# Performance work log

Hardware: AMD Instinct MI355X
Metric: run time of the kernel (lower is better)

## Reference

```python
import jax, jax.numpy as jnp
import numpy as np

N = 50000      # nodes
E = 800000     # edges (before self-loops)
H = 4          # heads
C = 32         # hidden per head (hidden*heads = 128); out_channels = 32
IN = 128
NEG_SLOPE = 0.2


def setup_inputs() -> dict:
    key = jax.random.key(0)
    ks = jax.random.split(key, 16)
    s = 0.1
    d = {
        "x": jax.random.normal(ks[0], (N, IN), jnp.float32),
        "edge_index": jax.random.randint(ks[1], (2, E), 0, N),
        "edge_type": jax.random.randint(ks[2], (E,), 0, 38),
        "node_type": jax.random.randint(ks[3], (N,), 0, 4),
        # layer 1: in=128 -> H*C, concat
        "W1": jax.random.normal(ks[4], (IN, H * C), jnp.float32) * s,
        "a1s": jax.random.normal(ks[5], (H, C), jnp.float32) * s,
        "a1d": jax.random.normal(ks[6], (H, C), jnp.float32) * s,
        "b1": jnp.zeros((H * C,), jnp.float32),
        # layer 2: H*C -> H*C, concat
        "W2": jax.random.normal(ks[7], (H * C, H * C), jnp.float32) * s,
        "a2s": jax.random.normal(ks[8], (H, C), jnp.float32) * s,
        "a2d": jax.random.normal(ks[9], (H, C), jnp.float32) * s,
        "b2": jnp.zeros((H * C,), jnp.float32),
        # layer 3: H*C -> C, heads=1, mean (concat=False)
        "W3": jax.random.normal(ks[10], (H * C, C), jnp.float32) * s,
        "a3s": jax.random.normal(ks[11], (1, C), jnp.float32) * s,
        "a3d": jax.random.normal(ks[12], (1, C), jnp.float32) * s,
        "b3": jnp.zeros((C,), jnp.float32),
    }
    return d


def gat_layer(x, src, dst, W, a_s, a_d, b, heads, concat):
    # PyG GATConv (eval mode): linear, per-edge attention logits, segment
    # softmax over incoming edges at dst, weighted scatter-sum, bias.
    h = (x @ W).reshape(N, heads, -1)            # [N, H, C]
    al_s = jnp.einsum('nhc,hc->nh', h, a_s)       # [N, H]
    al_d = jnp.einsum('nhc,hc->nh', h, a_d)
    e = jax.nn.leaky_relu(al_s[src] + al_d[dst], NEG_SLOPE)   # [E', H]
    m = jax.ops.segment_max(e, dst, num_segments=N)            # [N, H]
    p = jnp.exp(e - m[dst])
    z = jax.ops.segment_sum(p, dst, num_segments=N)            # [N, H]
    alpha = p / (z[dst] + 1e-16)                               # [E', H]
    out = jax.ops.segment_sum(h[src] * alpha[..., None], dst, num_segments=N)  # [N, H, C]
    out = out.reshape(N, -1) if concat else out.mean(axis=1)
    return out + b


def reference(x, edge_index, edge_type, node_type,
              W1, a1s, a1d, b1, W2, a2s, a2d, b2, W3, a3s, a3d, b3):
    # add self-loops (PyG GATConv default add_self_loops=True)
    loop = jnp.arange(N, dtype=edge_index.dtype)
    src = jnp.concatenate([edge_index[0], loop])
    dst = jnp.concatenate([edge_index[1], loop])
    h = gat_layer(x, src, dst, W1, a1s, a1d, b1, H, True)
    h = jax.nn.elu(h)
    h = gat_layer(h, src, dst, W2, a2s, a2d, b2, H, True)
    h = jax.nn.elu(h)
    out = gat_layer(h, src, dst, W3, a3s, a3d, b3, 1, False)
    return out
```

## Files before the change

### kernel.cpp

```cpp
#include <hip/hip_runtime.h>
#include <hip/hip_fp16.h>

#define LRELU_SLOPE 0.2f
#define BSH 8
#define EPB 3584
#define BCAP 5120
#define NSH 6

typedef _Float16 f16x8 __attribute__((ext_vector_type(8)));
typedef float f32x4 __attribute__((ext_vector_type(4)));

__device__ __forceinline__ float lrelu(float x) { return x >= 0.0f ? x : LRELU_SLOPE * x; }

__device__ __forceinline__ float sel4(float a, float b, float c, float d, int h) {
  float r = a;
  r = (h == 1) ? b : r;
  r = (h == 2) ? c : r;
  r = (h == 3) ? d : r;
  return r;
}


__device__ __forceinline__ void prep_one(const float* __restrict__ W, __half* __restrict__ out,
                                         int NT, int t) {
  int l = t & 63, f = t >> 6;
  int kt = f / NT, nt = f % NT;
  int k0 = kt * 32 + (l >> 4) * 8;
  int col = nt * 16 + (l & 15);
  union { __half h[8]; float4 v; } u;
#pragma unroll
  for (int j = 0; j < 8; ++j) u.h[j] = (__half)W[(size_t)(k0 + j) * (NT * 16) + col];
  *(float4*)(out + (size_t)t * 8) = u.v;
}

__global__ __launch_bounds__(256) void k_init(
    int* __restrict__ gcur,
    const float* __restrict__ W1, __half* __restrict__ wf1,
    const float* __restrict__ W2, __half* __restrict__ wf2,
    const float* __restrict__ W3, __half* __restrict__ wf3) {
  if (blockIdx.x == 0) {
    gcur[threadIdx.x] = threadIdx.x * BCAP;
    return;
  }
  int t = (blockIdx.x - 1) * 256 + threadIdx.x;
  if (t < 2048) prep_one(W1, wf1, 8, t);
  else if (t < 4096) prep_one(W2, wf2, 8, t - 2048);
  else if (t < 4608) prep_one(W3, wf3, 2, t - 4096);
}


__device__ __forceinline__ f16x8 load_a(const float* xp) {
  float4 lo = *(const float4*)xp;
  float4 hi = *(const float4*)(xp + 4);
  f16x8 a;
  a[0] = (_Float16)lo.x; a[1] = (_Float16)lo.y; a[2] = (_Float16)lo.z; a[3] = (_Float16)lo.w;
  a[4] = (_Float16)hi.x; a[5] = (_Float16)hi.y; a[6] = (_Float16)hi.z; a[7] = (_Float16)hi.w;
  return a;
}

__device__ __forceinline__ f16x8 load_a(const __half* xp) {
  return *(const f16x8*)xp;
}

template <int NT, int NH, typename IN, typename OUT>
__device__ __forceinline__ void gemm_body(
    const IN* __restrict__ x, const __half* __restrict__ wfrag,
    const float* __restrict__ a_s, const float* __restrict__ a_d,
    OUT* __restrict__ h, float* __restrict__ als, float* __restrict__ ald,
    int n, int ntiles, int tile, int lane) {
  const f16x8* wf = (const f16x8*)wfrag;
  f16x8 B[4][NT];
#pragma unroll
  for (int kt = 0; kt < 4; ++kt)
#pragma unroll
    for (int nt = 0; nt < NT; ++nt) B[kt][nt] = wf[(kt * NT + nt) * 64 + lane];
  if (tile >= ntiles) return;
  int r0 = tile * 16;
  int arow = r0 + (lane & 15);
  const IN* xp = x + (size_t)arow * 128 + (lane >> 4) * 8;
  bool full = (r0 + 16 <= n);
  f16x8 A[4];
#pragma unroll
  for (int kt = 0; kt < 4; ++kt) {
    if (full || arow < n) A[kt] = load_a(xp + kt * 32);
    else A[kt] = (f16x8){};
  }
  f32x4 acc[NT];
#pragma unroll
  for (int nt = 0; nt < NT; ++nt) acc[nt] = (f32x4){0.f, 0.f, 0.f, 0.f};
#pragma unroll
  for (int kt = 0; kt < 4; ++kt)
#pragma unroll
    for (int nt = 0; nt < NT; ++nt)
      acc[nt] = __builtin_amdgcn_mfma_f32_16x16x32_f16(A[kt], B[kt][nt], acc[nt], 0, 0, 0);
  int cb = lane & 15, rb = (lane >> 4) * 4;
  float asv[NT], adv[NT];
#pragma unroll
  for (int nt = 0; nt < NT; ++nt) {
    asv[nt] = a_s[nt * 16 + cb];
    adv[nt] = a_d[nt * 16 + cb];
  }
#pragma unroll
  for (int r = 0; r < 4; ++r) {
    int row = r0 + rb + r;
    if (!full && row >= n) break;
#pragma unroll
    for (int nt = 0; nt < NT; ++nt)
      h[(size_t)row * (NT * 16) + nt * 16 + cb] = (OUT)acc[nt][r];
    if (NH == 4) {
      float ps[4], pd[4];
#pragma unroll
      for (int hh = 0; hh < 4; ++hh) {
        ps[hh] = acc[2 * hh][r] * asv[2 * hh] + acc[2 * hh + 1][r] * asv[2 * hh + 1];
        pd[hh] = acc[2 * hh][r] * adv[2 * hh] + acc[2 * hh + 1][r] * adv[2 * hh + 1];
      }
#pragma unroll
      for (int off = 1; off < 16; off <<= 1) {
#pragma unroll
        for (int hh = 0; hh < 4; ++hh) {
          ps[hh] += __shfl_xor(ps[hh], off);
          pd[hh] += __shfl_xor(pd[hh], off);
        }
      }
      if (cb < 4) {
        als[row * 4 + cb] = sel4(ps[0], ps[1], ps[2], ps[3], cb);
        ald[row * 4 + cb] = sel4(pd[0], pd[1], pd[2], pd[3], cb);
      }
    } else {
      float ps = acc[0][r] * asv[0] + acc[1][r] * asv[1];
      float pd = acc[0][r] * adv[0] + acc[1][r] * adv[1];
#pragma unroll
      for (int off = 1; off < 16; off <<= 1) {
        ps += __shfl_xor(ps, off);
        pd += __shfl_xor(pd, off);
      }
      if (cb == 0) { als[row] = ps; ald[row] = pd; }
    }
  }
}

template <int NT, int NH, typename IN, typename OUT>
__global__ __launch_bounds__(256, 2) void gemm_mfma(
    const IN* __restrict__ x, const __half* __restrict__ wfrag,
    const float* __restrict__ a_s, const float* __restrict__ a_d,
    OUT* __restrict__ h, float* __restrict__ als, float* __restrict__ ald,
    int n, int ntiles) {
  int lane = threadIdx.x & 63, w = threadIdx.x >> 6;
  gemm_body<NT, NH, IN, OUT>(x, wfrag, a_s, a_d, h, als, ald, n, ntiles,
                             blockIdx.x * 4 + w, lane);
}


__global__ __launch_bounds__(256) void k_bucket_gemm(
    const int* __restrict__ ei, int E, int* __restrict__ gcur, int* __restrict__ ebuck,
    int bblocks,
    const float* __restrict__ x, const __half* __restrict__ wf1,
    const float* __restrict__ a1s, const float* __restrict__ a1d,
    __half* __restrict__ hA, float* __restrict__ als, float* __restrict__ ald,
    int n, int ntiles) {
  __shared__ int stage[EPB];
  __shared__ unsigned char bucket8[EPB];
  __shared__ int cnt[256], offs[256], gbase[256], curl[256], sm[256];
  if (blockIdx.x >= bblocks) {
    int lane = threadIdx.x & 63, w = threadIdx.x >> 6;
    gemm_body<8, 4, float, __half>(x, wf1, a1s, a1d, hA, als, ald, n, ntiles,
                                   (blockIdx.x - bblocks) * 4 + w, lane);
    return;
  }
  int t = threadIdx.x;
  int base = blockIdx.x * EPB;
  int count = E - base;
  if (count > EPB) count = EPB;
  if (count < 0) count = 0;
  cnt[t] = 0;
  __syncthreads();
  for (int i = t; i < count; i += 256) {
    int d = ei[E + base + i];
    atomicAdd(&cnt[d >> BSH], 1);
  }
  __syncthreads();
  sm[t] = cnt[t];
  __syncthreads();
#pragma unroll
  for (int off = 1; off < 256; off <<= 1) {
    int u = (t >= off) ? sm[t - off] : 0;
    __syncthreads();
    sm[t] += u;
    __syncthreads();
  }
  offs[t] = sm[t] - cnt[t];
  curl[t] = sm[t] - cnt[t];
  if (cnt[t] > 0) gbase[t] = atomicAdd(&gcur[t], cnt[t]);
  __syncthreads();
  for (int i = t; i < count; i += 256) {
    int s = ei[base + i];
    int d = ei[E + base + i];
    int b = d >> BSH;
    int r = atomicAdd(&curl[b], 1);
    stage[r] = (s << 8) | (d & 255);
    bucket8[r] = (unsigned char)b;
  }
  __syncthreads();
  for (int i = t; i < count; i += 256) {
    int b = bucket8[i];
    ebuck[gbase[b] + (i - offs[b])] = stage[i];
  }
}


__global__ __launch_bounds__(256) void k_fine_gemm(
    const int* __restrict__ ebuck, const int* __restrict__ gcur,
    int* __restrict__ rowend, int* __restrict__ colx, int n, int fineBlocks,
    const float* __restrict__ x, const __half* __restrict__ wf1,
    const float* __restrict__ a1s, const float* __restrict__ a1d,
    __half* __restrict__ hA, float* __restrict__ als, float* __restrict__ ald,
    int ntiles, int tile0) {
  if (blockIdx.x >= fineBlocks) {
    int lane = threadIdx.x & 63, w = threadIdx.x >> 6;
    gemm_body<8, 4, float, __half>(x, wf1, a1s, a1d, hA, als, ald, n, ntiles,
                                   tile0 + (blockIdx.x - fineBlocks) * 4 + w, lane);
    return;
  }
  __shared__ int cur[256];
  int b = blockIdx.x, t = threadIdx.x;
  int lo = b << BSH;
  int hi = lo + 256;
  if (hi > n) hi = n;
  int nn = hi - lo;
  cur[t] = (lo + t) << NSH;
  __syncthreads();
  int ebeg = b * BCAP, eend = gcur[b];
  for (int i = ebeg + t; i < eend; i += 256) {
    int p = ebuck[i];
    int pos = atomicAdd(&cur[p & 255], 1);
    colx[pos] = p >> 8;
  }
  __syncthreads();
  if (t < nn) rowend[lo + t] = cur[t];
}


__global__ __launch_bounds__(256) void k_agg128(
    const __half* __restrict__ h, const float* __restrict__ als,
    const float* __restrict__ ald, const int* __restrict__ rowend,
    const int* __restrict__ colx, const float* __restrict__ bias,
    __half* __restrict__ out, int n) {
  int w = threadIdx.x >> 6, lane = threadIdx.x & 63;
  int node = blockIdx.x * 4 + w;
  if (node >= n) return;
  int g = lane >> 3, q = lane & 7, head = q >> 1;
  int beg = node << NSH, end = rowend[node];
  float adh = ald[node * 4 + head];
  float acc[16] = {};
  float z = 0.f;
  int c0 = q * 16;
  if (g == 0) {
    float ws = __expf(lrelu(als[node * 4 + head] + adh));
    z = ws;
    float4 ra = *(const float4*)(h + (size_t)node * 128 + c0);
    float4 rb = *(const float4*)(h + (size_t)node * 128 + c0 + 8);
    const __half2* ha = (const __half2*)&ra;
    const __half2* hb = (const __half2*)&rb;
#pragma unroll
    for (int j = 0; j < 4; ++j) {
      float2 fa = __half22float2(ha[j]);
      float2 fb = __half22float2(hb[j]);
      acc[2 * j] = ws * fa.x;
      acc[2 * j + 1] = ws * fa.y;
      acc[8 + 2 * j] = ws * fb.x;
      acc[8 + 2 * j + 1] = ws * fb.y;
    }
  }
  for (int e = beg + g; e < end; e += 8) {
    int s = colx[e];
    float wv = __expf(lrelu(als[s * 4 + head] + adh));
    float4 ra = *(const float4*)(h + (size_t)s * 128 + c0);
    float4 rb = *(const float4*)(h + (size_t)s * 128 + c0 + 8);
    const __half2* ha = (const __half2*)&ra;
    const __half2* hb = (const __half2*)&rb;
    z += wv;
#pragma unroll
    for (int j = 0; j < 4; ++j) {
      float2 fa = __half22float2(ha[j]);
      float2 fb = __half22float2(hb[j]);
      acc[2 * j] = fmaf(wv, fa.x, acc[2 * j]);
      acc[2 * j + 1] = fmaf(wv, fa.y, acc[2 * j + 1]);
      acc[8 + 2 * j] = fmaf(wv, fb.x, acc[8 + 2 * j]);
      acc[8 + 2 * j + 1] = fmaf(wv, fb.y, acc[8 + 2 * j + 1]);
    }
  }
#pragma unroll
  for (int off = 8; off <= 32; off <<= 1) {
    z += __shfl_xor(z, off);
#pragma unroll
    for (int j = 0; j < 16; ++j) acc[j] += __shfl_xor(acc[j], off);
  }
  if (g == 0) {
    float inv = 1.f / z;
    union { __half h8[8]; float4 v; } ua, ub;
#pragma unroll
    for (int j = 0; j < 8; ++j) {
      float va = acc[j] * inv + bias[c0 + j];
      va = (va > 0.f) ? va : (__expf(va) - 1.f);
      ua.h8[j] = (__half)va;
      float vb = acc[8 + j] * inv + bias[c0 + 8 + j];
      vb = (vb > 0.f) ? vb : (__expf(vb) - 1.f);
      ub.h8[j] = (__half)vb;
    }
    *(float4*)&out[(size_t)node * 128 + c0] = ua.v;
    *(float4*)&out[(size_t)node * 128 + c0 + 8] = ub.v;
  }
}


__global__ __launch_bounds__(256) void k_agg32(
    const __half* __restrict__ h, const float* __restrict__ als,
    const float* __restrict__ ald, const int* __restrict__ rowend,
    const int* __restrict__ colx, const float* __restrict__ bias,
    float* __restrict__ out, int n) {
  int w = threadIdx.x >> 6, lane = threadIdx.x & 63;
  int node = blockIdx.x * 4 + w;
  if (node >= n) return;
  int g = lane >> 3, q = lane & 7;
  int beg = node << NSH, end = rowend[node];
  float ad = ald[node];
  float acc[4] = {};
  float z = 0.f;
  int c0 = q * 4;
  if (g == 0) {
    float ws = __expf(lrelu(als[node] + ad));
    float2 raw = *(const float2*)(h + (size_t)node * 32 + c0);
    const __half2* hh = (const __half2*)&raw;
    z = ws;
#pragma unroll
    for (int j = 0; j < 2; ++j) {
      float2 f = __half22float2(hh[j]);
      acc[2 * j] = ws * f.x;
      acc[2 * j + 1] = ws * f.y;
    }
  }
  for (int e = beg + g; e < end; e += 8) {
    int s = colx[e];
    float wv = __expf(lrelu(als[s] + ad));
    float2 raw = *(const float2*)(h + (size_t)s * 32 + c0);
    const __half2* hh = (const __half2*)&raw;
    z += wv;
#pragma unroll
    for (int j = 0; j < 2; ++j) {
      float2 f = __half22float2(hh[j]);
      acc[2 * j] = fmaf(wv, f.x, acc[2 * j]);
      acc[2 * j + 1] = fmaf(wv, f.y, acc[2 * j + 1]);
    }
  }
#pragma unroll
  for (int off = 8; off <= 32; off <<= 1) {
    z += __shfl_xor(z, off);
#pragma unroll
    for (int j = 0; j < 4; ++j) acc[j] += __shfl_xor(acc[j], off);
  }
  if (g == 0) {
    float inv = 1.f / z;
    float4 o;
    o.x = acc[0] * inv + bias[c0];
    o.y = acc[1] * inv + bias[c0 + 1];
    o.z = acc[2] * inv + bias[c0 + 2];
    o.w = acc[3] * inv + bias[c0 + 3];
    *(float4*)&out[(size_t)node * 32 + c0] = o;
  }
}


extern "C" void kernel_launch(void* const* d_in, const int* in_sizes, int n_in,
                              void* d_out, int out_size, void* d_ws, size_t ws_size,
                              hipStream_t stream) {
  const float* x   = (const float*)d_in[0];
  const int*   ei  = (const int*)d_in[1];
  const float* W1  = (const float*)d_in[4];
  const float* a1s = (const float*)d_in[5];
  const float* a1d = (const float*)d_in[6];
  const float* b1  = (const float*)d_in[7];
  const float* W2  = (const float*)d_in[8];
  const float* a2s = (const float*)d_in[9];
  const float* a2d = (const float*)d_in[10];
  const float* b2  = (const float*)d_in[11];
  const float* W3  = (const float*)d_in[12];
  const float* a3s = (const float*)d_in[13];
  const float* a3d = (const float*)d_in[14];
  const float* b3  = (const float*)d_in[15];
  const int N = in_sizes[0] / 128;
  const int E = in_sizes[1] / 2;
  const int ntiles = (N + 15) / 16;
  const int nbuck = (N + 255) >> BSH;

  char* ws = (char*)d_ws;
  size_t off = 0;
  auto alloc = [&](size_t bytes) -> void* {
    void* p = ws + off;
    off += (bytes + 255) & ~(size_t)255;
    return p;
  };
  __half* hA    = (__half*)alloc((size_t)N * 128 * 2);
  __half* hB    = (__half*)alloc((size_t)N * 128 * 2);
  __half* h32   = (__half*)alloc((size_t)N * 32 * 2);
  float*  als_a = (float*)alloc((size_t)N * 4 * 4);
  float*  ald_a = (float*)alloc((size_t)N * 4 * 4);
  float*  als_b = (float*)alloc((size_t)N * 4 * 4);
  float*  ald_b = (float*)alloc((size_t)N * 4 * 4);
  float*  als1  = (float*)alloc((size_t)N * 4);
  float*  ald1  = (float*)alloc((size_t)N * 4);
  int* rowend   = (int*)alloc((size_t)N * 4);
  int* gcur     = (int*)alloc(256 * 4);
  int* ebuck    = (int*)alloc((size_t)nbuck * BCAP * 4);
  int* colx     = (int*)alloc(((size_t)N << NSH) * 4);
  __half* wf1   = (__half*)alloc(4 * 8 * 64 * 8 * 2);
  __half* wf2   = (__half*)alloc(4 * 8 * 64 * 8 * 2);
  __half* wf3   = (__half*)alloc(4 * 2 * 64 * 8 * 2);
  (void)ws_size; (void)n_in; (void)out_size;

  k_init<<<19, 256, 0, stream>>>(gcur, W1, wf1, W2, wf2, W3, wf3);

  int gblk = (ntiles + 3) / 4;
  int bblocks = (E + EPB - 1) / EPB;
  int g1a = (gblk * 3) / 5;
  int g1b = gblk - g1a;
  int tile0 = g1a * 4;

  k_bucket_gemm<<<bblocks + g1a, 256, 0, stream>>>(ei, E, gcur, ebuck, bblocks,
                                                   x, wf1, a1s, a1d, hA, als_a, ald_a,
                                                   N, ntiles);
  k_fine_gemm<<<nbuck + g1b, 256, 0, stream>>>(ebuck, gcur, rowend, colx, N, nbuck,
                                               x, wf1, a1s, a1d, hA, als_a, ald_a,
                                               ntiles, tile0);

  k_agg128<<<(N + 3) / 4, 256, 0, stream>>>(hA, als_a, ald_a, rowend, colx, b1, hB, N);
  gemm_mfma<8, 4, __half, __half><<<gblk, 256, 0, stream>>>(hB, wf2, a2s, a2d, hA,
                                                            als_b, ald_b, N, ntiles);
  k_agg128<<<(N + 3) / 4, 256, 0, stream>>>(hA, als_b, ald_b, rowend, colx, b2, hB, N);
  gemm_mfma<2, 1, __half, __half><<<gblk, 256, 0, stream>>>(hB, wf3, a3s, a3d, h32,
                                                            als1, ald1, N, ntiles);
  k_agg32<<<(N + 3) / 4, 256, 0, stream>>>(h32, als1, ald1, rowend, colx, b3,
                                           (float*)d_out, N);
}
```

Baseline: 156.2 us.

## Fuse attention aggregation with the following layer GEMM in one kernel

Replaces the separate aggregation and MFMA GEMM kernels for layers 2 and 3 with a fused kernel. Each 1024-thread block aggregates 16 nodes, one wave per node, into an LDS tile. It then runs the next layer's MFMA projection from LDS, splits K across two wave groups reduced through shared memory, and computes the attention logits for that layer. This removes the global write and re-read of the intermediate activations and two launches, at the cost of a large block size, extra syncthreads, and idle waves during the GEMM phase.

```diff
diff --git a/kernel.cpp b/kernel.cpp
--- a/kernel.cpp
+++ b/kernel.cpp
@@ -58,15 +58,11 @@
   return a;
 }
 
-__device__ __forceinline__ f16x8 load_a(const __half* xp) {
-  return *(const f16x8*)xp;
-}
-
-template <int NT, int NH, typename IN, typename OUT>
+template <int NT, int NH>
 __device__ __forceinline__ void gemm_body(
-    const IN* __restrict__ x, const __half* __restrict__ wfrag,
+    const float* __restrict__ x, const __half* __restrict__ wfrag,
     const float* __restrict__ a_s, const float* __restrict__ a_d,
-    OUT* __restrict__ h, float* __restrict__ als, float* __restrict__ ald,
+    __half* __restrict__ h, float* __restrict__ als, float* __restrict__ ald,
     int n, int ntiles, int tile, int lane) {
   const f16x8* wf = (const f16x8*)wfrag;
   f16x8 B[4][NT];
@@ -77,7 +73,7 @@
   if (tile >= ntiles) return;
   int r0 = tile * 16;
   int arow = r0 + (lane & 15);
-  const IN* xp = x + (size_t)arow * 128 + (lane >> 4) * 8;
+  const float* xp = x + (size_t)arow * 128 + (lane >> 4) * 8;
   bool full = (r0 + 16 <= n);
   f16x8 A[4];
 #pragma unroll
@@ -106,48 +102,26 @@
     if (!full && row >= n) break;
 #pragma unroll
     for (int nt = 0; nt < NT; ++nt)
-      h[(size_t)row * (NT * 16) + nt * 16 + cb] = (OUT)acc[nt][r];
-    if (NH == 4) {
-      float ps[4], pd[4];
+      h[(size_t)row * (NT * 16) + nt * 16 + cb] = (__half)acc[nt][r];
+    float ps[4], pd[4];
+#pragma unroll
+    for (int hh = 0; hh < 4; ++hh) {
+      ps[hh] = acc[2 * hh][r] * asv[2 * hh] + acc[2 * hh + 1][r] * asv[2 * hh + 1];
+      pd[hh] = acc[2 * hh][r] * adv[2 * hh] + acc[2 * hh + 1][r] * adv[2 * hh + 1];
+    }
+#pragma unroll
+    for (int off = 1; off < 16; off <<= 1) {
 #pragma unroll
       for (int hh = 0; hh < 4; ++hh) {
-        ps[hh] = acc[2 * hh][r] * asv[2 * hh] + acc[2 * hh + 1][r] * asv[2 * hh + 1];
-        pd[hh] = acc[2 * hh][r] * adv[2 * hh] + acc[2 * hh + 1][r] * adv[2 * hh + 1];
-      }
-#pragma unroll
-      for (int off = 1; off < 16; off <<= 1) {
-#pragma unroll
-        for (int hh = 0; hh < 4; ++hh) {
-          ps[hh] += __shfl_xor(ps[hh], off);
-          pd[hh] += __shfl_xor(pd[hh], off);
-        }
-      }
-      if (cb < 4) {
-        als[row * 4 + cb] = sel4(ps[0], ps[1], ps[2], ps[3], cb);
-        ald[row * 4 + cb] = sel4(pd[0], pd[1], pd[2], pd[3], cb);
-      }
-    } else {
-      float ps = acc[0][r] * asv[0] + acc[1][r] * asv[1];
-      float pd = acc[0][r] * adv[0] + acc[1][r] * adv[1];
-#pragma unroll
-      for (int off = 1; off < 16; off <<= 1) {
-        ps += __shfl_xor(ps, off);
-        pd += __shfl_xor(pd, off);
-      }
-      if (cb == 0) { als[row] = ps; ald[row] = pd; }
-    }
-  }
-}
-
-template <int NT, int NH, typename IN, typename OUT>
-__global__ __launch_bounds__(256, 2) void gemm_mfma(
-    const IN* __restrict__ x, const __half* __restrict__ wfrag,
-    const float* __restrict__ a_s, const float* __restrict__ a_d,
-    OUT* __restrict__ h, float* __restrict__ als, float* __restrict__ ald,
-    int n, int ntiles) {
-  int lane = threadIdx.x & 63, w = threadIdx.x >> 6;
-  gemm_body<NT, NH, IN, OUT>(x, wfrag, a_s, a_d, h, als, ald, n, ntiles,
-                             blockIdx.x * 4 + w, lane);
+        ps[hh] += __shfl_xor(ps[hh], off);
+        pd[hh] += __shfl_xor(pd[hh], off);
+      }
+    }
+    if (cb < 4) {
+      als[row * 4 + cb] = sel4(ps[0], ps[1], ps[2], ps[3], cb);
+      ald[row * 4 + cb] = sel4(pd[0], pd[1], pd[2], pd[3], cb);
+    }
+  }
 }
 
 
@@ -163,8 +137,8 @@
   __shared__ int cnt[256], offs[256], gbase[256], curl[256], sm[256];
   if (blockIdx.x >= bblocks) {
     int lane = threadIdx.x & 63, w = threadIdx.x >> 6;
-    gemm_body<8, 4, float, __half>(x, wf1, a1s, a1d, hA, als, ald, n, ntiles,
-                                   (blockIdx.x - bblocks) * 4 + w, lane);
+    gemm_body<8, 4>(x, wf1, a1s, a1d, hA, als, ald, n, ntiles,
+                    (blockIdx.x - bblocks) * 4 + w, lane);
     return;
   }
   int t = threadIdx.x;
@@ -217,8 +191,8 @@
     int ntiles, int tile0) {
   if (blockIdx.x >= fineBlocks) {
     int lane = threadIdx.x & 63, w = threadIdx.x >> 6;
-    gemm_body<8, 4, float, __half>(x, wf1, a1s, a1d, hA, als, ald, n, ntiles,
-                                   tile0 + (blockIdx.x - fineBlocks) * 4 + w, lane);
+    gemm_body<8, 4>(x, wf1, a1s, a1d, hA, als, ald, n, ntiles,
+                    tile0 + (blockIdx.x - fineBlocks) * 4 + w, lane);
     return;
   }
   __shared__ int cur[256];
@@ -240,75 +214,162 @@
 }
 
 
-__global__ __launch_bounds__(256) void k_agg128(
-    const __half* __restrict__ h, const float* __restrict__ als,
-    const float* __restrict__ ald, const int* __restrict__ rowend,
+template <int NT, int NHO>
+__global__ __launch_bounds__(1024, 8) void agg_gemm(
+    const __half* __restrict__ hin, const float* __restrict__ als_in,
+    const float* __restrict__ ald_in, const int* __restrict__ rowend,
     const int* __restrict__ colx, const float* __restrict__ bias,
-    __half* __restrict__ out, int n) {
-  int w = threadIdx.x >> 6, lane = threadIdx.x & 63;
-  int node = blockIdx.x * 4 + w;
-  if (node >= n) return;
+    const __half* __restrict__ wfrag, const float* __restrict__ a_s,
+    const float* __restrict__ a_d, __half* __restrict__ hout,
+    float* __restrict__ als_out, float* __restrict__ ald_out, int n) {
+  __shared__ _Float16 tile[16][136];
+  __shared__ float redbuf[NT][16][17];
+  __shared__ float lps[NT][16], lpd[NT][16];
+  int tid = threadIdx.x;
+  int wv = tid >> 6, lane = tid & 63;
+  int base = blockIdx.x * 16;
+  int node = base + wv;
   int g = lane >> 3, q = lane & 7, head = q >> 1;
-  int beg = node << NSH, end = rowend[node];
-  float adh = ald[node * 4 + head];
-  float acc[16] = {};
-  float z = 0.f;
   int c0 = q * 16;
-  if (g == 0) {
-    float ws = __expf(lrelu(als[node * 4 + head] + adh));
-    z = ws;
-    float4 ra = *(const float4*)(h + (size_t)node * 128 + c0);
-    float4 rb = *(const float4*)(h + (size_t)node * 128 + c0 + 8);
-    const __half2* ha = (const __half2*)&ra;
-    const __half2* hb = (const __half2*)&rb;
-#pragma unroll
-    for (int j = 0; j < 4; ++j) {
-      float2 fa = __half22float2(ha[j]);
-      float2 fb = __half22float2(hb[j]);
-      acc[2 * j] = ws * fa.x;
-      acc[2 * j + 1] = ws * fa.y;
-      acc[8 + 2 * j] = ws * fb.x;
-      acc[8 + 2 * j + 1] = ws * fb.y;
-    }
-  }
-  for (int e = beg + g; e < end; e += 8) {
-    int s = colx[e];
-    float wv = __expf(lrelu(als[s * 4 + head] + adh));
-    float4 ra = *(const float4*)(h + (size_t)s * 128 + c0);
-    float4 rb = *(const float4*)(h + (size_t)s * 128 + c0 + 8);
-    const __half2* ha = (const __half2*)&ra;
-    const __half2* hb = (const __half2*)&rb;
-    z += wv;
-#pragma unroll
-    for (int j = 0; j < 4; ++j) {
-      float2 fa = __half22float2(ha[j]);
-      float2 fb = __half22float2(hb[j]);
-      acc[2 * j] = fmaf(wv, fa.x, acc[2 * j]);
-      acc[2 * j + 1] = fmaf(wv, fa.y, acc[2 * j + 1]);
-      acc[8 + 2 * j] = fmaf(wv, fb.x, acc[8 + 2 * j]);
-      acc[8 + 2 * j + 1] = fmaf(wv, fb.y, acc[8 + 2 * j + 1]);
-    }
-  }
-#pragma unroll
-  for (int off = 8; off <= 32; off <<= 1) {
-    z += __shfl_xor(z, off);
-#pragma unroll
-    for (int j = 0; j < 16; ++j) acc[j] += __shfl_xor(acc[j], off);
-  }
-  if (g == 0) {
-    float inv = 1.f / z;
-    union { __half h8[8]; float4 v; } ua, ub;
-#pragma unroll
-    for (int j = 0; j < 8; ++j) {
-      float va = acc[j] * inv + bias[c0 + j];
-      va = (va > 0.f) ? va : (__expf(va) - 1.f);
-      ua.h8[j] = (__half)va;
-      float vb = acc[8 + j] * inv + bias[c0 + 8 + j];
-      vb = (vb > 0.f) ? vb : (__expf(vb) - 1.f);
-      ub.h8[j] = (__half)vb;
-    }
-    *(float4*)&out[(size_t)node * 128 + c0] = ua.v;
-    *(float4*)&out[(size_t)node * 128 + c0 + 8] = ub.v;
+
+  if (node < n) {
+    int beg = node << NSH, end = rowend[node];
+    float adh = ald_in[node * 4 + head];
+    float acc[16] = {};
+    float z = 0.f;
+    if (g == 0) {
+      float ws = __expf(lrelu(als_in[node * 4 + head] + adh));
+      z = ws;
+      float4 ra = *(const float4*)(hin + (size_t)node * 128 + c0);
+      float4 rb = *(const float4*)(hin + (size_t)node * 128 + c0 + 8);
+      const __half2* ha = (const __half2*)&ra;
+      const __half2* hb = (const __half2*)&rb;
+#pragma unroll
+      for (int j = 0; j < 4; ++j) {
+        float2 fa = __half22float2(ha[j]);
+        float2 fb = __half22float2(hb[j]);
+        acc[2 * j] = ws * fa.x;
+        acc[2 * j + 1] = ws * fa.y;
+        acc[8 + 2 * j] = ws * fb.x;
+        acc[8 + 2 * j + 1] = ws * fb.y;
+      }
+    }
+    for (int e = beg + g; e < end; e += 8) {
+      int s = colx[e];
+      float wv2 = __expf(lrelu(als_in[s * 4 + head] + adh));
+      float4 ra = *(const float4*)(hin + (size_t)s * 128 + c0);
+      float4 rb = *(const float4*)(hin + (size_t)s * 128 + c0 + 8);
+      const __half2* ha = (const __half2*)&ra;
+      const __half2* hb = (const __half2*)&rb;
+      z += wv2;
+#pragma unroll
+      for (int j = 0; j < 4; ++j) {
+        float2 fa = __half22float2(ha[j]);
+        float2 fb = __half22float2(hb[j]);
+        acc[2 * j] = fmaf(wv2, fa.x, acc[2 * j]);
+        acc[2 * j + 1] = fmaf(wv2, fa.y, acc[2 * j + 1]);
+        acc[8 + 2 * j] = fmaf(wv2, fb.x, acc[8 + 2 * j]);
+        acc[8 + 2 * j + 1] = fmaf(wv2, fb.y, acc[8 + 2 * j + 1]);
+      }
+    }
+#pragma unroll
+    for (int off = 8; off <= 32; off <<= 1) {
+      z += __shfl_xor(z, off);
+#pragma unroll
+      for (int j = 0; j < 16; ++j) acc[j] += __shfl_xor(acc[j], off);
+    }
+    if (g == 0) {
+      float inv = 1.f / z;
+      f16x8 oa, ob;
+#pragma unroll
+      for (int j = 0; j < 8; ++j) {
+        float va = acc[j] * inv + bias[c0 + j];
+        va = (va > 0.f) ? va : (__expf(va) - 1.f);
+        oa[j] = (_Float16)va;
+        float vb = acc[8 + j] * inv + bias[c0 + 8 + j];
+        vb = (vb > 0.f) ? vb : (__expf(vb) - 1.f);
+        ob[j] = (_Float16)vb;
+      }
+      *(f16x8*)&tile[wv][c0] = oa;
+      *(f16x8*)&tile[wv][c0 + 8] = ob;
+    }
+  } else if (g == 0) {
+    f16x8 zz = {};
+    *(f16x8*)&tile[wv][c0] = zz;
+    *(f16x8*)&tile[wv][c0 + 8] = zz;
+  }
+  __syncthreads();
+
+  constexpr int ACT = (NT == 8) ? 16 : 4;
+  bool active = wv < ACT;
+  int ct = (NT == 8) ? (wv & 7) : (wv & 1);
+  int kh = (NT == 8) ? (wv >> 3) : ((wv >> 1) & 1);
+  int cb = lane & 15, rb4 = (lane >> 4) * 4;
+  f32x4 acc2 = (f32x4){0.f, 0.f, 0.f, 0.f};
+  if (active) {
+    const f16x8* wf = (const f16x8*)wfrag;
+    int arow = lane & 15;
+    int koff = kh * 64 + (lane >> 4) * 8;
+#pragma unroll
+    for (int kt = 0; kt < 2; ++kt) {
+      f16x8 A = *(const f16x8*)&tile[arow][koff + kt * 32];
+      f16x8 B = wf[((kh * 2 + kt) * NT + ct) * 64 + lane];
+      acc2 = __builtin_amdgcn_mfma_f32_16x16x32_f16(A, B, acc2, 0, 0, 0);
+    }
+    if (kh == 1) {
+#pragma unroll
+      for (int r = 0; r < 4; ++r) redbuf[ct][rb4 + r][cb] = acc2[r];
+    }
+  }
+  __syncthreads();
+  if (active && kh == 0) {
+#pragma unroll
+    for (int r = 0; r < 4; ++r) acc2[r] += redbuf[ct][rb4 + r][cb];
+    float asv = a_s[ct * 16 + cb], adv = a_d[ct * 16 + cb];
+    bool full = (base + 16 <= n);
+    float ps[4], pd[4];
+#pragma unroll
+    for (int r = 0; r < 4; ++r) {
+      int row = base + rb4 + r;
+      if (full || row < n)
+        hout[(size_t)row * (NT * 16) + ct * 16 + cb] = (__half)acc2[r];
+      ps[r] = acc2[r] * asv;
+      pd[r] = acc2[r] * adv;
+    }
+#pragma unroll
+    for (int off = 1; off < 16; off <<= 1) {
+#pragma unroll
+      for (int r = 0; r < 4; ++r) {
+        ps[r] += __shfl_xor(ps[r], off);
+        pd[r] += __shfl_xor(pd[r], off);
+      }
+    }
+    if (cb == 0) {
+#pragma unroll
+      for (int r = 0; r < 4; ++r) {
+        lps[ct][rb4 + r] = ps[r];
+        lpd[ct][rb4 + r] = pd[r];
+      }
+    }
+  }
+  __syncthreads();
+  if (wv == 0) {
+    if (NHO == 4) {
+      int row = lane >> 2, h = lane & 3;
+      int nd = base + row;
+      if (nd < n) {
+        als_out[nd * 4 + h] = lps[2 * h][row] + lps[2 * h + 1][row];
+        ald_out[nd * 4 + h] = lpd[2 * h][row] + lpd[2 * h + 1][row];
+      }
+    } else {
+      if (lane < 16) {
+        int nd = base + lane;
+        if (nd < n) {
+          als_out[nd] = lps[0][lane] + lps[1][lane];
+          ald_out[nd] = lpd[0][lane] + lpd[1][lane];
+        }
+      }
+    }
   }
 }
 
@@ -400,7 +461,7 @@
     return p;
   };
   __half* hA    = (__half*)alloc((size_t)N * 128 * 2);
-  __half* hB    = (__half*)alloc((size_t)N * 128 * 2);
+  __half* hA2   = (__half*)alloc((size_t)N * 128 * 2);
   __half* h32   = (__half*)alloc((size_t)N * 32 * 2);
   float*  als_a = (float*)alloc((size_t)N * 4 * 4);
   float*  ald_a = (float*)alloc((size_t)N * 4 * 4);
@@ -432,12 +493,11 @@
                                                x, wf1, a1s, a1d, hA, als_a, ald_a,
                                                ntiles, tile0);
 
-  k_agg128<<<(N + 3) / 4, 256, 0, stream>>>(hA, als_a, ald_a, rowend, colx, b1, hB, N);
-  gemm_mfma<8, 4, __half, __half><<<gblk, 256, 0, stream>>>(hB, wf2, a2s, a2d, hA,
-                                                            als_b, ald_b, N, ntiles);
-  k_agg128<<<(N + 3) / 4, 256, 0, stream>>>(hA, als_b, ald_b, rowend, colx, b2, hB, N);
-  gemm_mfma<2, 1, __half, __half><<<gblk, 256, 0, stream>>>(hB, wf3, a3s, a3d, h32,
-                                                            als1, ald1, N, ntiles);
+  int fblk = (N + 15) / 16;
+  agg_gemm<8, 4><<<fblk, 1024, 0, stream>>>(hA, als_a, ald_a, rowend, colx, b1,
+                                            wf2, a2s, a2d, hA2, als_b, ald_b, N);
+  agg_gemm<2, 1><<<fblk, 1024, 0, stream>>>(hA2, als_b, ald_b, rowend, colx, b2,
+                                            wf3, a3s, a3d, h32, als1, ald1, N);
   k_agg32<<<(N + 3) / 4, 256, 0, stream>>>(h32, als1, ald1, rowend, colx, b3,
                                            (float*)d_out, N);
 }
```

New measurement: 170.8 us. +9.3%, slower.

## Store hidden features in 16-column slabs and split aggregation per slab

Applied to the files above, without the earlier changes.

Hidden features for layers 1 and 2 are now written as eight slabs, each holding a 16-column slice for all nodes. Attention logits move to a head-major layout. The 128-wide aggregation kernel is replaced by one that launches eight times as many blocks, each gathering one 32-byte slab row per edge, so the gathered working set per launch fits better in cache. In exchange, every block re-reads the edge list and logits and recomputes exp for its slab, which multiplies index and exp work by eight.

```diff
diff --git a/kernel.cpp b/kernel.cpp
--- a/kernel.cpp
+++ b/kernel.cpp
@@ -58,15 +58,11 @@
   return a;
 }
 
-__device__ __forceinline__ f16x8 load_a(const __half* xp) {
-  return *(const f16x8*)xp;
-}
-
-template <int NT, int NH, typename IN, typename OUT>
+template <int NT, int NH, bool SIN, bool SOUT, typename IN>
 __device__ __forceinline__ void gemm_body(
     const IN* __restrict__ x, const __half* __restrict__ wfrag,
     const float* __restrict__ a_s, const float* __restrict__ a_d,
-    OUT* __restrict__ h, float* __restrict__ als, float* __restrict__ ald,
+    __half* __restrict__ h, float* __restrict__ als, float* __restrict__ ald,
     int n, int ntiles, int tile, int lane) {
   const f16x8* wf = (const f16x8*)wfrag;
   f16x8 B[4][NT];
@@ -77,13 +73,22 @@
   if (tile >= ntiles) return;
   int r0 = tile * 16;
   int arow = r0 + (lane & 15);
-  const IN* xp = x + (size_t)arow * 128 + (lane >> 4) * 8;
   bool full = (r0 + 16 <= n);
+  bool rowok = full || arow < n;
+  int l4 = lane >> 4;
   f16x8 A[4];
 #pragma unroll
   for (int kt = 0; kt < 4; ++kt) {
-    if (full || arow < n) A[kt] = load_a(xp + kt * 32);
-    else A[kt] = (f16x8){};
+    if (rowok) {
+      if constexpr (SIN) {
+        const __half* hp = (const __half*)x;
+        A[kt] = *(const f16x8*)(hp + ((size_t)(kt * 2 + (l4 >> 1)) * n + arow) * 16 + (l4 & 1) * 8);
+      } else {
+        A[kt] = load_a(x + (size_t)arow * 128 + l4 * 8 + kt * 32);
+      }
+    } else {
+      A[kt] = (f16x8){};
+    }
   }
   f32x4 acc[NT];
 #pragma unroll
@@ -93,7 +98,7 @@
 #pragma unroll
     for (int nt = 0; nt < NT; ++nt)
       acc[nt] = __builtin_amdgcn_mfma_f32_16x16x32_f16(A[kt], B[kt][nt], acc[nt], 0, 0, 0);
-  int cb = lane & 15, rb = (lane >> 4) * 4;
+  int cb = lane & 15, rb = l4 * 4;
   float asv[NT], adv[NT];
 #pragma unroll
   for (int nt = 0; nt < NT; ++nt) {
@@ -105,8 +110,12 @@
     int row = r0 + rb + r;
     if (!full && row >= n) break;
 #pragma unroll
-    for (int nt = 0; nt < NT; ++nt)
-      h[(size_t)row * (NT * 16) + nt * 16 + cb] = (OUT)acc[nt][r];
+    for (int nt = 0; nt < NT; ++nt) {
+      if constexpr (SOUT)
+        h[((size_t)nt * n + row) * 16 + cb] = (__half)acc[nt][r];
+      else
+        h[(size_t)row * (NT * 16) + nt * 16 + cb] = (__half)acc[nt][r];
+    }
     if (NH == 4) {
       float ps[4], pd[4];
 #pragma unroll
@@ -123,8 +132,8 @@
         }
       }
       if (cb < 4) {
-        als[row * 4 + cb] = sel4(ps[0], ps[1], ps[2], ps[3], cb);
-        ald[row * 4 + cb] = sel4(pd[0], pd[1], pd[2], pd[3], cb);
+        als[(size_t)cb * n + row] = sel4(ps[0], ps[1], ps[2], ps[3], cb);
+        ald[(size_t)cb * n + row] = sel4(pd[0], pd[1], pd[2], pd[3], cb);
       }
     } else {
       float ps = acc[0][r] * asv[0] + acc[1][r] * asv[1];
@@ -139,15 +148,15 @@
   }
 }
 
-template <int NT, int NH, typename IN, typename OUT>
+template <int NT, int NH, bool SIN, bool SOUT, typename IN>
 __global__ __launch_bounds__(256, 2) void gemm_mfma(
     const IN* __restrict__ x, const __half* __restrict__ wfrag,
     const float* __restrict__ a_s, const float* __restrict__ a_d,
-    OUT* __restrict__ h, float* __restrict__ als, float* __restrict__ ald,
+    __half* __restrict__ h, float* __restrict__ als, float* __restrict__ ald,
     int n, int ntiles) {
   int lane = threadIdx.x & 63, w = threadIdx.x >> 6;
-  gemm_body<NT, NH, IN, OUT>(x, wfrag, a_s, a_d, h, als, ald, n, ntiles,
-                             blockIdx.x * 4 + w, lane);
+  gemm_body<NT, NH, SIN, SOUT, IN>(x, wfrag, a_s, a_d, h, als, ald, n, ntiles,
+                                   blockIdx.x * 4 + w, lane);
 }
 
 
@@ -163,8 +172,8 @@
   __shared__ int cnt[256], offs[256], gbase[256], curl[256], sm[256];
   if (blockIdx.x >= bblocks) {
     int lane = threadIdx.x & 63, w = threadIdx.x >> 6;
-    gemm_body<8, 4, float, __half>(x, wf1, a1s, a1d, hA, als, ald, n, ntiles,
-                                   (blockIdx.x - bblocks) * 4 + w, lane);
+    gemm_body<8, 4, false, true, float>(x, wf1, a1s, a1d, hA, als, ald, n, ntiles,
+                                        (blockIdx.x - bblocks) * 4 + w, lane);
     return;
   }
   int t = threadIdx.x;
@@ -217,8 +226,8 @@
     int ntiles, int tile0) {
   if (blockIdx.x >= fineBlocks) {
     int lane = threadIdx.x & 63, w = threadIdx.x >> 6;
-    gemm_body<8, 4, float, __half>(x, wf1, a1s, a1d, hA, als, ald, n, ntiles,
-                                   tile0 + (blockIdx.x - fineBlocks) * 4 + w, lane);
+    gemm_body<8, 4, false, true, float>(x, wf1, a1s, a1d, hA, als, ald, n, ntiles,
+                                        tile0 + (blockIdx.x - fineBlocks) * 4 + w, lane);
     return;
   }
   __shared__ int cur[256];
@@ -240,75 +249,52 @@
 }
 
 
-__global__ __launch_bounds__(256) void k_agg128(
+__global__ __launch_bounds__(256) void k_agg128s(
     const __half* __restrict__ h, const float* __restrict__ als,
     const float* __restrict__ ald, const int* __restrict__ rowend,
     const int* __restrict__ colx, const float* __restrict__ bias,
     __half* __restrict__ out, int n) {
-  int w = threadIdx.x >> 6, lane = threadIdx.x & 63;
-  int node = blockIdx.x * 4 + w;
+  int wv = threadIdx.x >> 6, lane = threadIdx.x & 63;
+  int cs = blockIdx.x & 7;
+  int node = (blockIdx.x >> 3) * 4 + wv;
   if (node >= n) return;
-  int g = lane >> 3, q = lane & 7, head = q >> 1;
+  int g = lane >> 3, q = lane & 7;
+  int head = cs >> 1;
+  const __half* hs = h + (size_t)cs * n * 16;
+  const float* alsh = als + (size_t)head * n;
   int beg = node << NSH, end = rowend[node];
-  float adh = ald[node * 4 + head];
-  float acc[16] = {};
-  float z = 0.f;
-  int c0 = q * 16;
+  float adh = ald[(size_t)head * n + node];
+  float z = 0.f, a0 = 0.f, a1 = 0.f;
   if (g == 0) {
-    float ws = __expf(lrelu(als[node * 4 + head] + adh));
+    float ws = __expf(lrelu(alsh[node] + adh));
+    float2 f = __half22float2(*(const __half2*)(hs + (size_t)node * 16 + 2 * q));
     z = ws;
-    float4 ra = *(const float4*)(h + (size_t)node * 128 + c0);
-    float4 rb = *(const float4*)(h + (size_t)node * 128 + c0 + 8);
-    const __half2* ha = (const __half2*)&ra;
-    const __half2* hb = (const __half2*)&rb;
-#pragma unroll
-    for (int j = 0; j < 4; ++j) {
-      float2 fa = __half22float2(ha[j]);
-      float2 fb = __half22float2(hb[j]);
-      acc[2 * j] = ws * fa.x;
-      acc[2 * j + 1] = ws * fa.y;
-      acc[8 + 2 * j] = ws * fb.x;
-      acc[8 + 2 * j + 1] = ws * fb.y;
-    }
+    a0 = ws * f.x;
+    a1 = ws * f.y;
   }
   for (int e = beg + g; e < end; e += 8) {
     int s = colx[e];
-    float wv = __expf(lrelu(als[s * 4 + head] + adh));
-    float4 ra = *(const float4*)(h + (size_t)s * 128 + c0);
-    float4 rb = *(const float4*)(h + (size_t)s * 128 + c0 + 8);
-    const __half2* ha = (const __half2*)&ra;
-    const __half2* hb = (const __half2*)&rb;
-    z += wv;
-#pragma unroll
-    for (int j = 0; j < 4; ++j) {
-      float2 fa = __half22float2(ha[j]);
-      float2 fb = __half22float2(hb[j]);
-      acc[2 * j] = fmaf(wv, fa.x, acc[2 * j]);
-      acc[2 * j + 1] = fmaf(wv, fa.y, acc[2 * j + 1]);
-      acc[8 + 2 * j] = fmaf(wv, fb.x, acc[8 + 2 * j]);
-      acc[8 + 2 * j + 1] = fmaf(wv, fb.y, acc[8 + 2 * j + 1]);
-    }
+    float w2 = __expf(lrelu(alsh[s] + adh));
+    float2 f = __half22float2(*(const __half2*)(hs + (size_t)s * 16 + 2 * q));
+    z += w2;
+    a0 = fmaf(w2, f.x, a0);
+    a1 = fmaf(w2, f.y, a1);
   }
 #pragma unroll
   for (int off = 8; off <= 32; off <<= 1) {
     z += __shfl_xor(z, off);
-#pragma unroll
-    for (int j = 0; j < 16; ++j) acc[j] += __shfl_xor(acc[j], off);
+    a0 += __shfl_xor(a0, off);
+    a1 += __shfl_xor(a1, off);
   }
   if (g == 0) {
     float inv = 1.f / z;
-    union { __half h8[8]; float4 v; } ua, ub;
-#pragma unroll
-    for (int j = 0; j < 8; ++j) {
-      float va = acc[j] * inv + bias[c0 + j];
-      va = (va > 0.f) ? va : (__expf(va) - 1.f);
-      ua.h8[j] = (__half)va;
-      float vb = acc[8 + j] * inv + bias[c0 + 8 + j];
-      vb = (vb > 0.f) ? vb : (__expf(vb) - 1.f);
-      ub.h8[j] = (__half)vb;
-    }
-    *(float4*)&out[(size_t)node * 128 + c0] = ua.v;
-    *(float4*)&out[(size_t)node * 128 + c0 + 8] = ub.v;
+    int c = cs * 16 + 2 * q;
+    float v0 = a0 * inv + bias[c];
+    v0 = (v0 > 0.f) ? v0 : (__expf(v0) - 1.f);
+    float v1 = a1 * inv + bias[c + 1];
+    v1 = (v1 > 0.f) ? v1 : (__expf(v1) - 1.f);
+    *(__half2*)(out + ((size_t)cs * n + node) * 16 + 2 * q) =
+        __float22half2_rn(make_float2(v0, v1));
   }
 }
 
@@ -432,12 +418,13 @@
                                                x, wf1, a1s, a1d, hA, als_a, ald_a,
                                                ntiles, tile0);
 
-  k_agg128<<<(N + 3) / 4, 256, 0, stream>>>(hA, als_a, ald_a, rowend, colx, b1, hB, N);
-  gemm_mfma<8, 4, __half, __half><<<gblk, 256, 0, stream>>>(hB, wf2, a2s, a2d, hA,
-                                                            als_b, ald_b, N, ntiles);
-  k_agg128<<<(N + 3) / 4, 256, 0, stream>>>(hA, als_b, ald_b, rowend, colx, b2, hB, N);
-  gemm_mfma<2, 1, __half, __half><<<gblk, 256, 0, stream>>>(hB, wf3, a3s, a3d, h32,
-                                                            als1, ald1, N, ntiles);
+  int aggblk = ((N + 3) / 4) * 8;
+  k_agg128s<<<aggblk, 256, 0, stream>>>(hA, als_a, ald_a, rowend, colx, b1, hB, N);
+  gemm_mfma<8, 4, true, true, __half><<<gblk, 256, 0, stream>>>(hB, wf2, a2s, a2d, hA,
+                                                                als_b, ald_b, N, ntiles);
+  k_agg128s<<<aggblk, 256, 0, stream>>>(hA, als_b, ald_b, rowend, colx, b2, hB, N);
+  gemm_mfma<2, 1, true, false, __half><<<gblk, 256, 0, stream>>>(hB, wf3, a3s, a3d, h32,
+                                                                 als1, ald1, N, ntiles);
   k_agg32<<<(N + 3) / 4, 256, 0, stream>>>(h32, als1, ald1, rowend, colx, b3,
                                            (float*)d_out, N);
 }
```

Result: slower. 329.3 us (+110.8%).
